# Optimization experiments

Hardware: AMD Instinct MI355X
Metric: run time of the kernel (lower is better)

## Reference

```python
import math
import jax, jax.numpy as jnp
import numpy as np

D_MODEL = 512
N_HEADS = 8
FACTOR = 1
B, L = 16, 2048


def setup_inputs() -> dict:
    key = jax.random.key(0)
    ks = jax.random.split(key, 12)
    d = D_MODEL
    inp = {
        'queries': jax.random.normal(ks[0], (B, L, d), dtype=jnp.float32),
        'keys':    jax.random.normal(ks[1], (B, L, d), dtype=jnp.float32),
        'values':  jax.random.normal(ks[2], (B, L, d), dtype=jnp.float32),
        # projection params (nn.Linear: y = x @ W.T + b)
        'Wq': jax.random.normal(ks[3], (d, d), dtype=jnp.float32) * 0.02,
        'bq': jnp.zeros((d,), dtype=jnp.float32),
        'Wk': jax.random.normal(ks[4], (d, d), dtype=jnp.float32) * 0.02,
        'bk': jnp.zeros((d,), dtype=jnp.float32),
        'Wv': jax.random.normal(ks[5], (d, d), dtype=jnp.float32) * 0.02,
        'bv': jnp.zeros((d,), dtype=jnp.float32),
        'Wo': jax.random.normal(ks[6], (d, d), dtype=jnp.float32) * 0.02,
        'bo': jnp.zeros((d,), dtype=jnp.float32),
    }
    return inp


def _autocorrelation(q, k, v):
    # q, k, v: [B, H, E, L]
    length = q.shape[-1]
    q_fft = jnp.fft.rfft(q, axis=-1)
    k_fft = jnp.fft.rfft(k, axis=-1)
    corr = jnp.fft.irfft(q_fft * jnp.conj(k_fft), n=length, axis=-1)  # [B,H,E,L]

    # time_delay_agg_training
    top_k = int(FACTOR * math.log(length))  # static
    mean_value = corr.mean(axis=(1, 2))            # [B, L]
    _, index = jax.lax.top_k(mean_value.mean(axis=0), top_k)  # [k], batch-shared delays
    weights = mean_value[:, index]                 # [B, k]
    tmp_corr = jax.nn.softmax(weights, axis=-1)    # [B, k]

    # roll(values, -delay) == values[..., (arange(L)+delay) % L]
    idx = (jnp.arange(length)[None, :] + index[:, None]) % length  # [k, L]
    patterns = v[..., idx]                         # [B, H, E, k, L]
    delays_agg = jnp.einsum('bhekl,bk->bhel', patterns, tmp_corr)  # [B,H,E,L]
    return delays_agg


def reference(queries, keys, values, Wq, bq, Wk, bk, Wv, bv, Wo, bo):
    Bb, Ll, d = queries.shape
    H = N_HEADS
    E = d // H
    # projections, then [B, L, H, E] -> [B, H, E, L]
    q = (queries @ Wq.T + bq).reshape(Bb, Ll, H, E).transpose(0, 2, 3, 1)
    k = (keys    @ Wk.T + bk).reshape(Bb, Ll, H, E).transpose(0, 2, 3, 1)
    v = (values  @ Wv.T + bv).reshape(Bb, Ll, H, E).transpose(0, 2, 3, 1)

    agg = _autocorrelation(q, k, v)                 # [B, H, E, L]
    out = agg.transpose(0, 3, 1, 2).reshape(Bb, Ll, H * E)  # [B, L, d]
    return out @ Wo.T + bo
```

## Files before the change

kernel.cpp:

```cpp
#include <hip/hip_runtime.h>


typedef _Float16 f16;
typedef _Float16 f16x8 __attribute__((ext_vector_type(8)));
typedef _Float16 f16x4 __attribute__((ext_vector_type(4)));
typedef float    f32x4 __attribute__((ext_vector_type(4)));

#define PSI(i) ((i) + ((i) >> 3))
#define TWI(j) ((j) + ((j) >> 4))

__device__ __forceinline__ float2 f2add(float2 a, float2 b) { return make_float2(a.x + b.x, a.y + b.y); }
__device__ __forceinline__ float2 f2sub(float2 a, float2 b) { return make_float2(a.x - b.x, a.y - b.y); }
__device__ __forceinline__ float2 cmul(float2 a, float2 b)  { return make_float2(a.x * b.x - a.y * b.y, a.x * b.y + a.y * b.x); }

__global__ __launch_bounds__(256) void cvt_inputs(
    const float* __restrict__ q, const float* __restrict__ k, const float* __restrict__ v,
    f16* __restrict__ xq, f16* __restrict__ xk, f16* __restrict__ xv)
{
    const float* src = (blockIdx.y == 0) ? q : (blockIdx.y == 1) ? k : v;
    f16*         dst = (blockIdx.y == 0) ? xq : (blockIdx.y == 1) ? xk : xv;
    const int i = blockIdx.x * 256 + threadIdx.x;
    float4 val = ((const float4*)src)[i];
    f16x4 h = { (f16)val.x, (f16)val.y, (f16)val.z, (f16)val.w };
    ((f16x4*)dst)[i] = h;
}

__global__ __launch_bounds__(256) void cvt_weights(
    const float* __restrict__ w0, const float* __restrict__ w1,
    const float* __restrict__ w2, const float* __restrict__ w3,
    f16* __restrict__ o0, f16* __restrict__ o1, f16* __restrict__ o2, f16* __restrict__ o3)
{
    const float* src = (blockIdx.y == 0) ? w0 : (blockIdx.y == 1) ? w1 : (blockIdx.y == 2) ? w2 : w3;
    f16*         dst = (blockIdx.y == 0) ? o0 : (blockIdx.y == 1) ? o1 : (blockIdx.y == 2) ? o2 : o3;
    const int i = blockIdx.x * 256 + threadIdx.x;
    float4 val = ((const float4*)src)[i];
    f16x4 h = { (f16)val.x, (f16)val.y, (f16)val.z, (f16)val.w };
    ((f16x4*)dst)[i] = h;
}

template<int NR>
__device__ __forceinline__ void stage_op(const f16* __restrict__ G, int row0, int k0,
                                         f16* __restrict__ lds, int tid)
{
#pragma unroll
    for (int q = 0; q < NR; ++q) {
        const int r = q * 64 + (tid >> 3);
        const int u = (tid & 7) ^ ((tid >> 3) & 7);
        const f16* g = G + (size_t)(row0 + r) * 512 + k0 + u * 8;
        f16* d = lds + q * 4096 + (tid >> 6) * 512;
        __builtin_amdgcn_global_load_lds(
            (const __attribute__((address_space(1))) void*)g,
            (__attribute__((address_space(3))) void*)d, 16, 0, 0);
    }
}

template<int F16OUT, int WM_L2, int MT_L2, int NT_L2, int SWZ, int SPLITB>
__global__ __launch_bounds__(512, 2) void gemm_nt(
    const f16* __restrict__ A0, const f16* __restrict__ B0, const f16* __restrict__ B1,
    void* __restrict__ Cout, int N,
    const float* __restrict__ bias_q, const float* __restrict__ bias_k,
    const float* __restrict__ bias_col)
{
    constexpr int WM = 1 << WM_L2;
    constexpr int WN = 8 >> WM_L2;
    constexpr int BM = WM * 64;
    constexpr int BN = WN * 64;
    constexpr int NKT = 8;
    constexpr int ESZ = F16OUT ? 2 : 4;
    static_assert(BM * BN * ESZ <= 3 * (BM + BN) * 64 * 2, "C tile must fit in staging LDS");

    __shared__ __align__(16) char smem[3 * (BM + BN) * 64 * 2];
    f16* smA = (f16*)smem;
    f16* smB = (f16*)smem + 3 * BM * 64;

    const int tid  = threadIdx.x;
    const int wave = tid >> 6, lane = tid & 63;

    int mt, nt;
    if (SWZ == 1) {
        const int xcd = blockIdx.x & 7, slot = blockIdx.x >> 3;
        mt = slot & ((1 << MT_L2) - 1);
        nt = (xcd << (NT_L2 - 3)) | (slot >> MT_L2);
    } else if (SWZ == 2) {
        const int xcd = blockIdx.x & 7, slot = blockIdx.x >> 3;
        nt = slot & ((1 << NT_L2) - 1);
        mt = (xcd << (MT_L2 - 3)) | (slot >> NT_L2);
    } else {
        nt = blockIdx.x & ((1 << NT_L2) - 1);
        mt = blockIdx.x >> NT_L2;
    }
    const int m0 = mt * BM, n0 = nt * BN;

    const bool useB1 = SPLITB && (mt >= (1 << (MT_L2 - 1)));
    const f16* Bg = useB1 ? B1 : B0;
    const float* brow = SPLITB
        ? (useB1 ? bias_k - (1 << (MT_L2 - 1)) * BM : bias_q)
        : bias_q;

    f32x4 acc[4][4];
#pragma unroll
    for (int m = 0; m < 4; ++m)
#pragma unroll
        for (int n = 0; n < 4; ++n) acc[m][n] = (f32x4){0.f, 0.f, 0.f, 0.f};

    const int fr = lane & 15;
    const int kg = (lane >> 4) * 8;
    const int rowm = fr & 7;
    const int wr = wave >> (3 - WM_L2);
    const int wc = wave & (WN - 1);
    const int warow = wr * 64 + fr;
    const int wbrow = wc * 64 + fr;

    auto compute = [&](const f16* __restrict__ Ab, const f16* __restrict__ Bb) {
#pragma unroll
        for (int k2 = 0; k2 < 2; ++k2) {
            const int kb = k2 * 32 + kg;
            const int col = ((kb >> 3) ^ rowm) << 3;
            f16x8 af[4], bf[4];
#pragma unroll
            for (int m = 0; m < 4; ++m) af[m] = *(const f16x8*)&Ab[(warow + m * 16) * 64 + col];
#pragma unroll
            for (int n = 0; n < 4; ++n) bf[n] = *(const f16x8*)&Bb[(wbrow + n * 16) * 64 + col];
#pragma unroll
            for (int m = 0; m < 4; ++m)
#pragma unroll
                for (int n = 0; n < 4; ++n)
                    acc[m][n] = __builtin_amdgcn_mfma_f32_16x16x32_f16(af[m], bf[n], acc[m][n], 0, 0, 0);
        }
    };

    stage_op<WM>(A0, m0, 0,  smA, tid);
    stage_op<WN>(Bg, n0, 0,  smB, tid);
    stage_op<WM>(A0, m0, 64, smA + BM * 64, tid);
    stage_op<WN>(Bg, n0, 64, smB + BN * 64, tid);
    asm volatile("s_waitcnt vmcnt(6)" ::: "memory");
    __builtin_amdgcn_s_barrier();

#pragma unroll 1
    for (int kk = 0; kk < NKT; ++kk) {
        const int cur = kk % 3;
        if (kk < NKT - 2) {
            const int nxt = (kk + 2) % 3;
            stage_op<WM>(A0, m0, (kk + 2) * 64, smA + nxt * BM * 64, tid);
            stage_op<WN>(Bg, n0, (kk + 2) * 64, smB + nxt * BN * 64, tid);
        }
        compute(smA + cur * BM * 64, smB + cur * BN * 64);
        if (kk < NKT - 2) {
            asm volatile("s_waitcnt vmcnt(6) lgkmcnt(0)" ::: "memory");
            __builtin_amdgcn_s_barrier();
        } else if (kk == NKT - 2) {
            asm volatile("s_waitcnt vmcnt(0) lgkmcnt(0)" ::: "memory");
            __builtin_amdgcn_s_barrier();
        }
    }

    __syncthreads();
    {
        char* CT = smem;
        const int lr0 = wr * 64 + ((lane >> 4) << 2);
        const int lc0 = wc * 64 + fr;
#pragma unroll
        for (int m = 0; m < 4; ++m)
#pragma unroll
            for (int n = 0; n < 4; ++n) {
                const int col = lc0 + n * 16;
                const float bc = bias_col ? bias_col[n0 + col] : 0.f;
#pragma unroll
                for (int j = 0; j < 4; ++j) {
                    const int row = lr0 + m * 16 + j;
                    float v = acc[m][n][j] + bc + (brow ? brow[m0 + row] : 0.f);
                    if (F16OUT) ((f16*)CT)[row * BN + col] = (f16)v;
                    else        ((float*)CT)[row * BN + col] = v;
                }
            }
        __syncthreads();
        constexpr int CPR = BN * ESZ / 16;
        constexpr int CHUNKS = BM * CPR;
#pragma unroll 1
        for (int i = tid; i < CHUNKS; i += 512) {
            const int row = i / CPR;
            const int off = (i % CPR) * 16;
            int4 vv = *(const int4*)(CT + i * 16);
            *(int4*)((char*)Cout + ((size_t)(m0 + row) * N + n0) * ESZ + off) = vv;
        }
    }
}

template<int S>
__device__ __forceinline__ void fft_pass2(float2* __restrict__ z, const float2* __restrict__ tw, int tid)
{
    constexpr int m = 1024 >> S;
    constexpr int h = m >> 1;
#pragma unroll
    for (int rep = 0; rep < 2; ++rep) {
        const int idx = tid + rep * 256;
        const int j2  = idx & (h - 1);
        const int blk = idx >> (9 - S);
        const int i   = (blk << (11 - S)) + j2;
        const float2 w1 = tw[TWI(j2 << S)];
        const float2 w2 = tw[TWI(j2 << (S + 1))];
        float2 a = z[PSI(i)], b = z[PSI(i + h)], c = z[PSI(i + m)], d = z[PSI(i + m + h)];
        float2 a1 = f2add(a, c);
        float2 c1 = cmul(f2sub(a, c), w1);
        float2 b1 = f2add(b, d);
        float2 t0 = cmul(f2sub(b, d), w1);
        float2 d1 = make_float2(t0.y, -t0.x);
        z[PSI(i)]         = f2add(a1, b1);
        z[PSI(i + h)]     = cmul(f2sub(a1, b1), w2);
        z[PSI(i + m)]     = f2add(c1, d1);
        z[PSI(i + m + h)] = cmul(f2sub(c1, d1), w2);
    }
    __syncthreads();
}

__device__ __forceinline__ void fft_tail_scatter(float2* __restrict__ z, int tid)
{
    float2 v[8];
    const int p0 = tid * 8;
#pragma unroll
    for (int e = 0; e < 8; ++e) v[e] = z[PSI(p0 + e)];
    __syncthreads();
    constexpr float RS = 0.70710678118654752f;
    const float2 W8[4] = { {1.f, 0.f}, {RS, -RS}, {0.f, -1.f}, {-RS, -RS} };
#pragma unroll
    for (int e = 0; e < 4; ++e) {
        float2 t = f2sub(v[e], v[e + 4]);
        v[e]     = f2add(v[e], v[e + 4]);
        v[e + 4] = cmul(t, W8[e]);
    }
#pragma unroll
    for (int base = 0; base < 8; base += 4) {
        float2 t0 = f2sub(v[base], v[base + 2]);
        v[base]     = f2add(v[base], v[base + 2]);
        v[base + 2] = t0;
        float2 t1 = f2sub(v[base + 1], v[base + 3]);
        v[base + 1] = f2add(v[base + 1], v[base + 3]);
        v[base + 3] = make_float2(t1.y, -t1.x);
    }
#pragma unroll
    for (int base = 0; base < 8; base += 2) {
        float2 t = f2sub(v[base], v[base + 1]);
        v[base]     = f2add(v[base], v[base + 1]);
        v[base + 1] = t;
    }
    const int br8t = (int)(__brev((unsigned)tid) >> 24);
    const int BR3[8] = {0, 4, 2, 6, 1, 5, 3, 7};
#pragma unroll
    for (int e = 0; e < 8; ++e) {
        const int f = br8t + (BR3[e] << 8);
        z[PSI(f)] = v[e];
    }
    __syncthreads();
}

__device__ __forceinline__ void fft2048_natural(float2* __restrict__ z, const float2* __restrict__ tw, int tid)
{
    fft_pass2<0>(z, tw, tid);
    fft_pass2<2>(z, tw, tid);
    fft_pass2<4>(z, tw, tid);
    fft_pass2<6>(z, tw, tid);
    fft_tail_scatter(z, tid);
}

__device__ __forceinline__ void fill_tw(float2* __restrict__ tw, int tid)
{
    for (int j = tid; j < 1024; j += 256) {
        float sv, cv;
        sincospif(-(float)j * (1.0f / 1024.0f), &sv, &cv);
        tw[TWI(j)] = make_float2(cv, sv);
    }
}

__global__ __launch_bounds__(256) void fft_corr(
    const f16* __restrict__ Qt, const f16* __restrict__ Kt,
    float2* __restrict__ Sp)
{
    __shared__ float2 z[2304];
    __shared__ float2 tw[1088];
    const int tid = threadIdx.x;
    const int grp = blockIdx.x;
    const int b   = blockIdx.y;

    fill_tw(tw, tid);
    float2 racc[5];
#pragma unroll
    for (int r = 0; r < 5; ++r) racc[r] = make_float2(0.f, 0.f);
    __syncthreads();

    for (int ch = 0; ch < 8; ++ch) {
        const int c = grp * 8 + ch;
        const f16x8* qr = (const f16x8*)(Qt + ((size_t)c * 16 + b) * 2048);
        const f16x8* kr = (const f16x8*)(Kt + ((size_t)c * 16 + b) * 2048);
        f16x8 qv = qr[tid], kv = kr[tid];
        const int e0 = tid * 8;
#pragma unroll
        for (int j = 0; j < 8; ++j)
            z[PSI(e0 + j)] = make_float2((float)qv[j], (float)kv[j]);
        __syncthreads();
        fft2048_natural(z, tw, tid);
#pragma unroll
        for (int r = 0; r < 5; ++r) {
            const int f = tid + (r << 8);
            if (f <= 1024) {
                const int pf = (2048 - f) & 2047;
                float2 Zf  = z[PSI(f)];
                float2 Zc0 = z[PSI(pf)];
                float qx = 0.5f * (Zf.x + Zc0.x), qy = 0.5f * (Zf.y - Zc0.y);
                float dx = Zf.x - Zc0.x,          dy = Zf.y + Zc0.y;
                float kx = 0.5f * dy,             ky = -0.5f * dx;
                racc[r].x += qx * kx + qy * ky;
                racc[r].y += qy * kx - qx * ky;
            }
        }
        __syncthreads();
    }
    float2* out = Sp + ((size_t)b * 64 + grp) * 1025;
#pragma unroll
    for (int r = 0; r < 5; ++r) {
        const int f = tid + (r << 8);
        if (f <= 1024) out[f] = racc[r];
    }
}

__global__ __launch_bounds__(256) void reduce_sp(
    const float2* __restrict__ Sp, float2* __restrict__ Sred)
{
    const int b = blockIdx.x;
    const int f = blockIdx.y * 256 + threadIdx.x;
    if (f > 1024) return;
    const float2* base = Sp + (size_t)b * 64 * 1025 + f;
    float sx = 0.f, sy = 0.f;
#pragma unroll 8
    for (int g = 0; g < 64; ++g) {
        float2 p = base[(size_t)g * 1025];
        sx += p.x; sy += p.y;
    }
    Sred[b * 1025 + f] = make_float2(sx, sy);
}

__global__ __launch_bounds__(256) void ifft_mean(
    const float2* __restrict__ Sred, float* __restrict__ mv)
{
    __shared__ float2 z[2304];
    __shared__ float2 tw[1088];
    const int tid = threadIdx.x;
    const int b   = blockIdx.x;
    fill_tw(tw, tid);
#pragma unroll
    for (int r = 0; r < 5; ++r) {
        const int f = tid + (r << 8);
        if (f <= 1024) {
            float2 s = Sred[b * 1025 + f];
            z[PSI(f)] = make_float2(s.x, -s.y);
            if (f >= 1 && f <= 1023)
                z[PSI(2048 - f)] = make_float2(s.x, s.y);
        }
    }
    __syncthreads();
    fft2048_natural(z, tw, tid);
    const float scale = 1.0f / (2048.0f * 512.0f);
    for (int t = tid; t < 2048; t += 256)
        mv[(size_t)b * 2048 + t] = z[PSI(t)].x * scale;
}

__global__ __launch_bounds__(256) void select_topk(
    const float* __restrict__ mv, int* __restrict__ sel, float* __restrict__ wsm)
{
    __shared__ float u[2048];
    __shared__ float rv[256];
    __shared__ int   ri[256];
    __shared__ int   ssel[7];
    const int tid = threadIdx.x;
    for (int t = tid; t < 2048; t += 256) {
        float s = 0.f;
        for (int b = 0; b < 16; ++b) s += mv[b * 2048 + t];
        u[t] = s;
    }
    __syncthreads();
    for (int k = 0; k < 7; ++k) {
        float best = -3.4e38f; int bi = 0x7fffffff;
        for (int t = tid; t < 2048; t += 256)
            if (u[t] > best) { best = u[t]; bi = t; }
        rv[tid] = best; ri[tid] = bi;
        __syncthreads();
        for (int off = 128; off > 0; off >>= 1) {
            if (tid < off) {
                if (rv[tid + off] > rv[tid] ||
                    (rv[tid + off] == rv[tid] && ri[tid + off] < ri[tid])) {
                    rv[tid] = rv[tid + off]; ri[tid] = ri[tid + off];
                }
            }
            __syncthreads();
        }
        if (tid == 0) { ssel[k] = ri[0]; sel[k] = ri[0]; u[ri[0]] = -3.4e38f; }
        __syncthreads();
    }
    if (tid < 16) {
        float vals[7], mx = -3.4e38f;
        for (int k = 0; k < 7; ++k) { vals[k] = mv[tid * 2048 + ssel[k]]; mx = fmaxf(mx, vals[k]); }
        float se = 0.f;
        for (int k = 0; k < 7; ++k) { vals[k] = expf(vals[k] - mx); se += vals[k]; }
        for (int k = 0; k < 7; ++k) wsm[tid * 7 + k] = vals[k] / se;
    }
}

__global__ __launch_bounds__(256) void aggregate(
    const f16* __restrict__ V, const int* __restrict__ sel,
    const float* __restrict__ wsm, f16* __restrict__ agg)
{
    __shared__ int   sidx[7];
    __shared__ float sw[7];
    const int bl = blockIdx.x;
    const int b = bl >> 11, l = bl & 2047;
    if (threadIdx.x < 7) { sidx[threadIdx.x] = sel[threadIdx.x]; sw[threadIdx.x] = wsm[b * 7 + threadIdx.x]; }
    __syncthreads();
    const int c = threadIdx.x;
    float a0 = 0.f, a1 = 0.f;
#pragma unroll
    for (int k = 0; k < 7; ++k) {
        const int lk = (l + sidx[k]) & 2047;
        const f16* row = V + ((size_t)b * 2048 + lk) * 512;
        a0 += sw[k] * (float)row[c];
        a1 += sw[k] * (float)row[c + 256];
    }
    f16* orow = agg + ((size_t)b * 2048 + l) * 512;
    orow[c]       = (f16)a0;
    orow[c + 256] = (f16)a1;
}

extern "C" void kernel_launch(void* const* d_in, const int* in_sizes, int n_in,
                              void* d_out, int out_size, void* d_ws, size_t ws_size,
                              hipStream_t stream)
{
    (void)in_sizes; (void)n_in; (void)out_size; (void)ws_size;
    const float* queries = (const float*)d_in[0];
    const float* keys    = (const float*)d_in[1];
    const float* values  = (const float*)d_in[2];
    const float* Wq = (const float*)d_in[3];
    const float* bq = (const float*)d_in[4];
    const float* Wk = (const float*)d_in[5];
    const float* bk = (const float*)d_in[6];
    const float* Wv = (const float*)d_in[7];
    const float* bv = (const float*)d_in[8];
    const float* Wo = (const float*)d_in[9];
    const float* bo = (const float*)d_in[10];

    char* p = (char*)d_ws;
    f16*    Xq  = (f16*)p;    p += 33554432;
    f16*    Xk  = (f16*)p;    p += 33554432;
    f16*    Xv  = (f16*)p;    p += 33554432;
    f16*    QKt = (f16*)p;    p += 67108864;
    f16*    Vb  = (f16*)p;    p += 33554432;
    f16*    agg = (f16*)p;    p += 33554432;
    f16*    wqh = (f16*)p;    p += 524288;
    f16*    wkh = (f16*)p;    p += 524288;
    f16*    wvh = (f16*)p;    p += 524288;
    f16*    woh = (f16*)p;    p += 524288;
    float2* Sp  = (float2*)p; p += 8396800;
    float2* Srd = (float2*)p; p += 131200;
    float*  mv  = (float*)p;  p += 131072;
    int*    sel = (int*)p;    p += 256;
    float*  wsm = (float*)p;  p += 512;
    f16*    Kt  = QKt + (size_t)512 * 32768;

    cvt_weights<<<dim3(256, 4), 256, 0, stream>>>(Wq, Wk, Wv, Wo, wqh, wkh, wvh, woh);
    cvt_inputs<<<dim3(16384, 3), 256, 0, stream>>>(queries, keys, values, Xq, Xk, Xv);

    gemm_nt<1, 1, 3, 7, 1, 1><<<1024, 512, 0, stream>>>(
        wqh, Xq, Xk, QKt, 32768, bq, bk, nullptr);

    gemm_nt<1, 2, 7, 2, 2, 0><<<512, 512, 0, stream>>>(
        Xv, wvh, nullptr, Vb, 512, nullptr, nullptr, bv);

    fft_corr<<<dim3(64, 16), 256, 0, stream>>>(QKt, Kt, Sp);
    reduce_sp<<<dim3(16, 5), 256, 0, stream>>>(Sp, Srd);
    ifft_mean<<<16, 256, 0, stream>>>(Srd, mv);
    select_topk<<<1, 256, 0, stream>>>(mv, sel, wsm);
    aggregate<<<32768, 256, 0, stream>>>(Vb, sel, wsm, agg);

    gemm_nt<0, 2, 7, 2, 2, 0><<<512, 512, 0, stream>>>(
        agg, woh, nullptr, (float*)d_out, 512, nullptr, nullptr, bo);
}
```

Measured before the change: 313.3 us.

## Enlarge GEMM tiles to 256x256 with double buffering and swizzled epilogue

The GEMM kernel moves from 128x256/256x128 tiles with triple-buffered 64-wide K stages to fixed 256x256 tiles, double-buffered across 128KB of LDS, and each wave now holds an 8x4 MFMA accumulator grid. The output staging uses an XOR-swizzled LDS layout to cut bank conflicts, and the fp32 output path is written in two halves so it fits in LDS. The goal is more data reuse per loaded tile and fewer blocks. In exchange it risks lower occupancy from the larger LDS and register footprint, and less load latency hiding with only two buffers. The input conversion kernel also now converts 8 elements per thread with wider stores.

```diff
diff --git a/kernel.cpp b/kernel.cpp
--- a/kernel.cpp
+++ b/kernel.cpp
@@ -20,9 +20,11 @@
     const float* src = (blockIdx.y == 0) ? q : (blockIdx.y == 1) ? k : v;
     f16*         dst = (blockIdx.y == 0) ? xq : (blockIdx.y == 1) ? xk : xv;
     const int i = blockIdx.x * 256 + threadIdx.x;
-    float4 val = ((const float4*)src)[i];
-    f16x4 h = { (f16)val.x, (f16)val.y, (f16)val.z, (f16)val.w };
-    ((f16x4*)dst)[i] = h;
+    float4 a = ((const float4*)src)[2 * i];
+    float4 b = ((const float4*)src)[2 * i + 1];
+    f16x8 h = { (f16)a.x, (f16)a.y, (f16)a.z, (f16)a.w,
+                (f16)b.x, (f16)b.y, (f16)b.z, (f16)b.w };
+    ((f16x8*)dst)[i] = h;
 }
 
 __global__ __launch_bounds__(256) void cvt_weights(
@@ -38,12 +40,11 @@
     ((f16x4*)dst)[i] = h;
 }
 
-template<int NR>
-__device__ __forceinline__ void stage_op(const f16* __restrict__ G, int row0, int k0,
-                                         f16* __restrict__ lds, int tid)
-{
-#pragma unroll
-    for (int q = 0; q < NR; ++q) {
+__device__ __forceinline__ void stage_op256(const f16* __restrict__ G, int row0, int k0,
+                                            f16* __restrict__ lds, int tid)
+{
+#pragma unroll
+    for (int q = 0; q < 4; ++q) {
         const int r = q * 64 + (tid >> 3);
         const int u = (tid & 7) ^ ((tid >> 3) & 7);
         const f16* g = G + (size_t)(row0 + r) * 512 + k0 + u * 8;
@@ -54,24 +55,19 @@
     }
 }
 
-template<int F16OUT, int WM_L2, int MT_L2, int NT_L2, int SWZ, int SPLITB>
+template<int F16OUT, int MT_L2, int NT_L2, int SWZ, int SPLITB>
 __global__ __launch_bounds__(512, 2) void gemm_nt(
     const f16* __restrict__ A0, const f16* __restrict__ B0, const f16* __restrict__ B1,
     void* __restrict__ Cout, int N,
     const float* __restrict__ bias_q, const float* __restrict__ bias_k,
     const float* __restrict__ bias_col)
 {
-    constexpr int WM = 1 << WM_L2;
-    constexpr int WN = 8 >> WM_L2;
-    constexpr int BM = WM * 64;
-    constexpr int BN = WN * 64;
-    constexpr int NKT = 8;
+    constexpr int BM = 256, BN = 256, NKT = 8;
     constexpr int ESZ = F16OUT ? 2 : 4;
-    static_assert(BM * BN * ESZ <= 3 * (BM + BN) * 64 * 2, "C tile must fit in staging LDS");
-
-    __shared__ __align__(16) char smem[3 * (BM + BN) * 64 * 2];
+
+    __shared__ __align__(16) char smem[131072];
     f16* smA = (f16*)smem;
-    f16* smB = (f16*)smem + 3 * BM * 64;
+    f16* smB = (f16*)smem + 2 * BM * 64;
 
     const int tid  = threadIdx.x;
     const int wave = tid >> 6, lane = tid & 63;
@@ -97,18 +93,18 @@
         ? (useB1 ? bias_k - (1 << (MT_L2 - 1)) * BM : bias_q)
         : bias_q;
 
-    f32x4 acc[4][4];
-#pragma unroll
-    for (int m = 0; m < 4; ++m)
+    f32x4 acc[8][4];
+#pragma unroll
+    for (int m = 0; m < 8; ++m)
 #pragma unroll
         for (int n = 0; n < 4; ++n) acc[m][n] = (f32x4){0.f, 0.f, 0.f, 0.f};
 
     const int fr = lane & 15;
     const int kg = (lane >> 4) * 8;
     const int rowm = fr & 7;
-    const int wr = wave >> (3 - WM_L2);
-    const int wc = wave & (WN - 1);
-    const int warow = wr * 64 + fr;
+    const int wr = wave >> 2;
+    const int wc = wave & 3;
+    const int warow = wr * 128 + fr;
     const int wbrow = wc * 64 + fr;
 
     auto compute = [&](const f16* __restrict__ Ab, const f16* __restrict__ Bb) {
@@ -116,72 +112,71 @@
         for (int k2 = 0; k2 < 2; ++k2) {
             const int kb = k2 * 32 + kg;
             const int col = ((kb >> 3) ^ rowm) << 3;
-            f16x8 af[4], bf[4];
-#pragma unroll
-            for (int m = 0; m < 4; ++m) af[m] = *(const f16x8*)&Ab[(warow + m * 16) * 64 + col];
+            f16x8 af[8], bf[4];
+#pragma unroll
+            for (int m = 0; m < 8; ++m) af[m] = *(const f16x8*)&Ab[(warow + m * 16) * 64 + col];
 #pragma unroll
             for (int n = 0; n < 4; ++n) bf[n] = *(const f16x8*)&Bb[(wbrow + n * 16) * 64 + col];
 #pragma unroll
-            for (int m = 0; m < 4; ++m)
+            for (int m = 0; m < 8; ++m)
 #pragma unroll
                 for (int n = 0; n < 4; ++n)
                     acc[m][n] = __builtin_amdgcn_mfma_f32_16x16x32_f16(af[m], bf[n], acc[m][n], 0, 0, 0);
         }
     };
 
-    stage_op<WM>(A0, m0, 0,  smA, tid);
-    stage_op<WN>(Bg, n0, 0,  smB, tid);
-    stage_op<WM>(A0, m0, 64, smA + BM * 64, tid);
-    stage_op<WN>(Bg, n0, 64, smB + BN * 64, tid);
-    asm volatile("s_waitcnt vmcnt(6)" ::: "memory");
+    stage_op256(A0, m0, 0, smA, tid);
+    stage_op256(Bg, n0, 0, smB, tid);
+    asm volatile("s_waitcnt vmcnt(0)" ::: "memory");
     __builtin_amdgcn_s_barrier();
 
 #pragma unroll 1
     for (int kk = 0; kk < NKT; ++kk) {
-        const int cur = kk % 3;
-        if (kk < NKT - 2) {
-            const int nxt = (kk + 2) % 3;
-            stage_op<WM>(A0, m0, (kk + 2) * 64, smA + nxt * BM * 64, tid);
-            stage_op<WN>(Bg, n0, (kk + 2) * 64, smB + nxt * BN * 64, tid);
+        const int cur = kk & 1;
+        if (kk < NKT - 1) {
+            stage_op256(A0, m0, (kk + 1) * 64, smA + (cur ^ 1) * BM * 64, tid);
+            stage_op256(Bg, n0, (kk + 1) * 64, smB + (cur ^ 1) * BN * 64, tid);
         }
         compute(smA + cur * BM * 64, smB + cur * BN * 64);
-        if (kk < NKT - 2) {
-            asm volatile("s_waitcnt vmcnt(6) lgkmcnt(0)" ::: "memory");
-            __builtin_amdgcn_s_barrier();
-        } else if (kk == NKT - 2) {
-            asm volatile("s_waitcnt vmcnt(0) lgkmcnt(0)" ::: "memory");
-            __builtin_amdgcn_s_barrier();
-        }
-    }
-
-    __syncthreads();
-    {
-        char* CT = smem;
-        const int lr0 = wr * 64 + ((lane >> 4) << 2);
-        const int lc0 = wc * 64 + fr;
-#pragma unroll
-        for (int m = 0; m < 4; ++m)
-#pragma unroll
-            for (int n = 0; n < 4; ++n) {
-                const int col = lc0 + n * 16;
-                const float bc = bias_col ? bias_col[n0 + col] : 0.f;
-#pragma unroll
-                for (int j = 0; j < 4; ++j) {
-                    const int row = lr0 + m * 16 + j;
-                    float v = acc[m][n][j] + bc + (brow ? brow[m0 + row] : 0.f);
-                    if (F16OUT) ((f16*)CT)[row * BN + col] = (f16)v;
-                    else        ((float*)CT)[row * BN + col] = v;
+        asm volatile("s_waitcnt vmcnt(0) lgkmcnt(0)" ::: "memory");
+        __builtin_amdgcn_s_barrier();
+    }
+
+    constexpr int L     = F16OUT ? 3 : 2;
+    constexpr int CPR   = (BN * ESZ) / 16;
+    constexpr int HROWS = F16OUT ? 256 : 128;
+    constexpr int NH    = F16OUT ? 1 : 2;
+#pragma unroll 1
+    for (int h = 0; h < NH; ++h) {
+        __syncthreads();
+        if (F16OUT || wr == h) {
+            const int lr0 = wr * 128 + ((lane >> 4) << 2);
+#pragma unroll
+            for (int m = 0; m < 8; ++m)
+#pragma unroll
+                for (int n = 0; n < 4; ++n) {
+                    const int col = wc * 64 + n * 16 + fr;
+                    const float bc = bias_col ? bias_col[n0 + col] : 0.f;
+#pragma unroll
+                    for (int j = 0; j < 4; ++j) {
+                        const int row  = lr0 + m * 16 + j;
+                        const int rl   = row - h * HROWS * (F16OUT ? 0 : 1);
+                        const int scol = ((((col >> L) ^ (row & 7)) << L) | (col & ((1 << L) - 1)));
+                        float v = acc[m][n][j] + bc + (brow ? brow[m0 + row] : 0.f);
+                        if (F16OUT) ((f16*)smem)[row * BN + scol] = (f16)v;
+                        else        ((float*)smem)[rl * BN + scol] = v;
+                    }
                 }
-            }
-        __syncthreads();
-        constexpr int CPR = BN * ESZ / 16;
-        constexpr int CHUNKS = BM * CPR;
+        }
+        __syncthreads();
+        const int chunks = HROWS * CPR;
 #pragma unroll 1
-        for (int i = tid; i < CHUNKS; i += 512) {
-            const int row = i / CPR;
-            const int off = (i % CPR) * 16;
-            int4 vv = *(const int4*)(CT + i * 16);
-            *(int4*)((char*)Cout + ((size_t)(m0 + row) * N + n0) * ESZ + off) = vv;
+        for (int i = tid; i < chunks; i += 512) {
+            const int rl  = i / CPR;
+            const int u   = i % CPR;
+            const int row = h * HROWS + rl;
+            int4 vv = *(const int4*)(smem + (rl * CPR + (u ^ (row & 7))) * 16);
+            *(int4*)((char*)Cout + ((size_t)(m0 + row) * N + n0) * ESZ + u * 16) = vv;
         }
     }
 }
@@ -464,12 +459,12 @@
     f16*    Kt  = QKt + (size_t)512 * 32768;
 
     cvt_weights<<<dim3(256, 4), 256, 0, stream>>>(Wq, Wk, Wv, Wo, wqh, wkh, wvh, woh);
-    cvt_inputs<<<dim3(16384, 3), 256, 0, stream>>>(queries, keys, values, Xq, Xk, Xv);
-
-    gemm_nt<1, 1, 3, 7, 1, 1><<<1024, 512, 0, stream>>>(
+    cvt_inputs<<<dim3(8192, 3), 256, 0, stream>>>(queries, keys, values, Xq, Xk, Xv);
+
+    gemm_nt<1, 2, 7, 1, 1><<<512, 512, 0, stream>>>(
         wqh, Xq, Xk, QKt, 32768, bq, bk, nullptr);
 
-    gemm_nt<1, 2, 7, 2, 2, 0><<<512, 512, 0, stream>>>(
+    gemm_nt<1, 7, 1, 2, 0><<<256, 512, 0, stream>>>(
         Xv, wvh, nullptr, Vb, 512, nullptr, nullptr, bv);
 
     fft_corr<<<dim3(64, 16), 256, 0, stream>>>(QKt, Kt, Sp);
@@ -478,6 +473,6 @@
     select_topk<<<1, 256, 0, stream>>>(mv, sel, wsm);
     aggregate<<<32768, 256, 0, stream>>>(Vb, sel, wsm, agg);
 
-    gemm_nt<0, 2, 7, 2, 2, 0><<<512, 512, 0, stream>>>(
+    gemm_nt<0, 7, 1, 2, 0><<<256, 512, 0, stream>>>(
         agg, woh, nullptr, (float*)d_out, 512, nullptr, nullptr, bo);
 }
```

Measured after the change: 318.4 us. No clear change (+1.6%).
